# Kernel optimization log

Hardware: AMD Instinct MI355X
Metric: run time of the kernel (lower is better)

## Reference

```python
import jax, jax.numpy as jnp
import numpy as np

B, T, C, H = 8, 2048, 1024, 64

def setup_inputs() -> dict:
    key = jax.random.key(0)
    kx, kq, kk, kv = jax.random.split(key, 4)
    scale = 1.0 / np.sqrt(C)
    return {
        "x": jax.random.normal(kx, (B, T, C), dtype=jnp.float32),
        "Wq": jax.random.normal(kq, (C, H), dtype=jnp.float32) * scale,
        "Wk": jax.random.normal(kk, (C, H), dtype=jnp.float32) * scale,
        "Wv": jax.random.normal(kv, (C, H), dtype=jnp.float32) * scale,
    }

def reference(x, Wq, Wk, Wv):
    # q,k,v: [B,T,H]
    q = jnp.einsum('btc,ch->bth', x, Wq)
    k = jnp.einsum('btc,ch->bth', x, Wk)
    v = jnp.einsum('btc,ch->bth', x, Wv)
    scale = k.shape[-1] ** -0.5
    wei = jnp.einsum('bth,bsh->bts', q, k) * scale  # [B,T,T]
    causal = jnp.tril(jnp.ones((x.shape[1], x.shape[1]), dtype=bool))
    wei = jnp.where(causal, wei, -jnp.inf)
    wei = jax.nn.softmax(wei, axis=-1)
    out = jnp.einsum('bts,bsh->bth', wei, v)  # [B,T,H]
    return out
```

## Files before the change

### kernel.cpp

```cpp
#include <hip/hip_runtime.h>

#define B_ 8
#define T_ 2048
#define C_ 1024
#define H_ 64

typedef __bf16 bf16x8 __attribute__((ext_vector_type(8)));
typedef float  f32x4  __attribute__((ext_vector_type(4)));
typedef unsigned short u16x8 __attribute__((ext_vector_type(8)));

__device__ __forceinline__ unsigned short f2bf(float f) {
    unsigned u = __builtin_bit_cast(unsigned, f);
    u += 0x8000u;
    return (unsigned short)(u >> 16);
}

__device__ __forceinline__ float bf2f(unsigned short v) {
    unsigned u = ((unsigned)v) << 16;
    return __builtin_bit_cast(float, u);
}

__device__ __forceinline__ unsigned pack2(float lo, float hi) {
    unsigned a = __builtin_bit_cast(unsigned, lo) + 0x8000u;
    unsigned b = __builtin_bit_cast(unsigned, hi) + 0x8000u;
    return (a >> 16) | (b & 0xffff0000u);
}

union U8 { unsigned u32[4]; u16x8 v; };

__device__ __forceinline__ u16x8 cvt8(float4 f0, float4 f1) {
    U8 r;
    r.u32[0] = pack2(f0.x, f0.y);
    r.u32[1] = pack2(f0.z, f0.w);
    r.u32[2] = pack2(f1.x, f1.y);
    r.u32[3] = pack2(f1.z, f1.w);
    return r.v;
}

__device__ __forceinline__ bf16x8 load8_bf(const unsigned short* p) {
    return __builtin_bit_cast(bf16x8, *(const u16x8*)p);
}

__device__ __forceinline__ void gload_lds16(const float* g, float* l) {
    __builtin_amdgcn_global_load_lds(
        (const __attribute__((address_space(1))) unsigned int*)g,
        (__attribute__((address_space(3))) unsigned int*)l, 16, 0, 0);
}

__device__ __forceinline__ void stage_rows(const float* __restrict__ x,
                                           float* lbuf, size_t rbase,
                                           int ns, int lane, int half) {
#pragma unroll
    for (int q = 0; q < 8; q++) {
        int jj  = half * 8 + q;
        int j   = ns * 16 + jj;
        int row = j >> 2;
        int S0  = (j & 3) * 64;
        int g   = (S0 + lane) ^ (row & 7);
        gload_lds16(x + (rbase + row) * C_ + (size_t)g * 4,
                    lbuf + row * 1024 + S0 * 4);
    }
}


__global__ void cast_weights(const float* __restrict__ Wq,
                             const float* __restrict__ Wk,
                             const float* __restrict__ Wv,
                             unsigned short* __restrict__ Wtf) {
    int idx = blockIdx.x * blockDim.x + threadIdx.x;
    int n   = idx % 192;
    int c   = idx / 192;
    int w   = n >> 6;
    int h   = n & 63;
    const float* W = (w == 0) ? Wq : (w == 1) ? Wk : Wv;
    int nt = n >> 4, l16 = n & 15;
    int kk = c >> 5, quad = (c >> 3) & 3, j = c & 7;
    Wtf[(size_t)(nt * 32 + kk) * 512 + l16 * 32 + quad * 8 + j] =
        f2bf(W[(size_t)c * H_ + h]);
}

__global__ __launch_bounds__(256, 1) void qkv_proj(
        const float* __restrict__ x,
        const unsigned short* __restrict__ Wtf,
        unsigned short* __restrict__ Qf,
        unsigned short* __restrict__ Kf,
        unsigned short* __restrict__ Vf) {
    __shared__ __attribute__((aligned(16))) float Axs[2][16 * 1024];
    __shared__ __attribute__((aligned(16))) unsigned short E[3072];

    const int tid  = threadIdx.x;
    const int ns   = tid >> 6;
    const int lane = tid & 63;
    const int l16  = lane & 15;
    const int quad = lane >> 4;
    const size_t rblk = (size_t)blockIdx.x * 64;
    const int bb   = (int)(rblk >> 11);
    const int xsw  = l16 & 7;
    const unsigned short* wp = Wtf + (size_t)(ns * 3 * 32) * 512
                               + l16 * 32 + quad * 8;

    stage_rows(x, Axs[0], rblk, ns, lane, 0);
    stage_rows(x, Axs[0], rblk, ns, lane, 1);
    __syncthreads();

    for (int t = 0; t < 4; t++) {
        const float* Arow = &Axs[t & 1][l16 * 1024];
        float* bufN = &Axs[(t + 1) & 1][0];
        const size_t rnext = rblk + (size_t)(t + 1) * 16;

        f32x4 acc[3];
#pragma unroll
        for (int i = 0; i < 3; i++) acc[i] = (f32x4){0.f, 0.f, 0.f, 0.f};

#pragma unroll
        for (int kc = 0; kc < 4; kc++) {
            if (kc == 1 && t < 3) stage_rows(x, bufN, rnext, ns, lane, 0);
            if (kc == 2 && t < 3) stage_rows(x, bufN, rnext, ns, lane, 1);
#pragma unroll
            for (int k8 = 0; k8 < 8; k8++) {
                const int kk = kc * 8 + k8;
                int g0 = kk * 8 + quad * 2;
                float4 f0 = *(const float4*)(Arow + (size_t)((g0    ) ^ xsw) * 4);
                float4 f1 = *(const float4*)(Arow + (size_t)((g0 + 1) ^ xsw) * 4);
                bf16x8 a0 = __builtin_bit_cast(bf16x8, cvt8(f0, f1));
#pragma unroll
                for (int i = 0; i < 3; i++) {
                    bf16x8 b = load8_bf(wp + (size_t)(i * 32 + kk) * 512);
                    acc[i] = __builtin_amdgcn_mfma_f32_16x16x32_bf16(a0, b, acc[i], 0, 0, 0);
                }
            }
        }

        __syncthreads();

        const int tloc0  = (int)((rblk + (size_t)t * 16) & (T_ - 1));
        const int t16_0  = tloc0 >> 4;
        const int s32    = tloc0 >> 5;
        const int half16 = t16_0 & 1;

#pragma unroll
        for (int i = 0; i < 3; i++) {
            int nt = ns * 3 + i;
#pragma unroll
            for (int r = 0; r < 4; r++) {
                unsigned short bv = f2bf(acc[i][r]);
                int off;
                if (nt < 4) {
                    off = (nt >> 1) * 512 + (quad * 4 + r) * 32 +
                          ((nt & 1) * 2 + (l16 >> 3)) * 8 + (l16 & 7);
                } else if (nt < 8) {
                    int nk = nt - 4;
                    off = 1024 + (nk >> 1) * 512 + (quad * 4 + r) * 32 +
                          ((nk & 1) * 2 + (l16 >> 3)) * 8 + (l16 & 7);
                } else {
                    int ht = nt - 8;
                    off = 2048 + ht * 256 + l16 * 16 + quad * 4 + r;
                }
                E[off] = bv;
            }
        }
        __syncthreads();

        {
            int ch = tid >> 6;
            int g  = tid & 63;
            unsigned short* dst = (ch < 2) ? Qf : Kf;
            int part = ch & 1;
            dst += ((size_t)(bb * 128 + t16_0) * 2 + part) * 512;
            *(u16x8*)(dst + g * 8) = *(const u16x8*)(&E[ch * 512 + g * 8]);
        }
        if (tid < 128) {
            int ht   = tid >> 5;
            int rr   = tid & 31;
            int l16v = rr >> 1;
            int hh   = rr & 1;
            unsigned short* dst = Vf + ((size_t)(bb * 64 + s32) * 4 + ht) * 512
                                  + l16v * 32 + half16 * 16 + hh * 8;
            *(u16x8*)dst = *(const u16x8*)(&E[2048 + ht * 256 + l16v * 16 + hh * 8]);
        }
    }
}

#define PROW 33
#define OMS2 66

__global__ __launch_bounds__(256) void attn(
        const unsigned short* __restrict__ Qf,
        const unsigned short* __restrict__ Kf,
        const unsigned short* __restrict__ Vf,
        float* __restrict__ out) {
    __shared__ unsigned int ps_[4 * 32 * PROW];
    __shared__ unsigned short Om_[4 * 32 * OMS2];
    __shared__ float mred_[4][32];
    __shared__ float lred_[4][32];

    const int tid  = threadIdx.x;
    const int wave = tid >> 6;
    const int lane = tid & 63;
    const int l16  = lane & 15;
    const int quad = lane >> 4;
    const int b    = blockIdx.x & 7;
    const int qt32 = blockIdx.x >> 3;
    const int q0   = qt32 * 32;
    const int tdiag = qt32 >> 1;

    const int loff = l16 * 32 + quad * 8;

    bf16x8 qf[2][2];
#pragma unroll
    for (int qg = 0; qg < 2; qg++) {
        const unsigned short* Qfb = Qf + (size_t)((b * 128 + qt32 * 2 + qg) * 2) * 512;
        qf[qg][0] = load8_bf(Qfb + loff);
        qf[qg][1] = load8_bf(Qfb + 512 + loff);
    }

    f32x4 o[8];
#pragma unroll
    for (int i = 0; i < 8; i++) o[i] = (f32x4){0.f, 0.f, 0.f, 0.f};
    float m_run[2] = {-1e30f, -1e30f}, l_run[2] = {0.f, 0.f};

    const float scale = 0.125f;
    const unsigned short* Kfb = Kf + (size_t)b * 128 * 1024;
    const unsigned short* Vfb = Vf + (size_t)b * 64 * 2048;
    unsigned int* Pw = &ps_[wave * 32 * PROW];

    for (int t = wave; t <= tdiag; t += 4) {
        bf16x8 vf[8];
#pragma unroll
        for (int ks = 0; ks < 2; ks++)
#pragma unroll
            for (int ht = 0; ht < 4; ht++)
                vf[ht * 2 + ks] = load8_bf(
                    Vfb + ((size_t)(t * 2 + ks) * 4 + ht) * 512 + loff);

        f32x4 s[2][4];
#pragma unroll
        for (int nt = 0; nt < 4; nt++) {
            const unsigned short* kp = Kfb + (size_t)(t * 4 + nt) * 1024;
            bf16x8 kf0 = load8_bf(kp + loff);
            bf16x8 kf1 = load8_bf(kp + 512 + loff);
#pragma unroll
            for (int qg = 0; qg < 2; qg++) {
                f32x4 z = (f32x4){0.f, 0.f, 0.f, 0.f};
                z = __builtin_amdgcn_mfma_f32_16x16x32_bf16(kf0, qf[qg][0], z, 0, 0, 0);
                z = __builtin_amdgcn_mfma_f32_16x16x32_bf16(kf1, qf[qg][1], z, 0, 0, 0);
                s[qg][nt] = z;
            }
        }

#pragma unroll
        for (int qg = 0; qg < 2; qg++)
#pragma unroll
            for (int nt = 0; nt < 4; nt++)
#pragma unroll
                for (int r = 0; r < 4; r++) s[qg][nt][r] *= scale;

        if (t == tdiag) {
#pragma unroll
            for (int qg = 0; qg < 2; qg++) {
                int q = q0 + qg * 16 + l16;
#pragma unroll
                for (int nt = 0; nt < 4; nt++)
#pragma unroll
                    for (int r = 0; r < 4; r++) {
                        int key = t * 64 + nt * 16 + quad * 4 + r;
                        if (key > q) s[qg][nt][r] = -1e30f;
                    }
            }
        }

#pragma unroll
        for (int qg = 0; qg < 2; qg++) {
            float m0 = fmaxf(fmaxf(s[qg][0][0], s[qg][0][1]), fmaxf(s[qg][0][2], s[qg][0][3]));
            float m1 = fmaxf(fmaxf(s[qg][1][0], s[qg][1][1]), fmaxf(s[qg][1][2], s[qg][1][3]));
            float m2 = fmaxf(fmaxf(s[qg][2][0], s[qg][2][1]), fmaxf(s[qg][2][2], s[qg][2][3]));
            float m3 = fmaxf(fmaxf(s[qg][3][0], s[qg][3][1]), fmaxf(s[qg][3][2], s[qg][3][3]));
            float mx = fmaxf(fmaxf(m0, m1), fmaxf(m2, m3));
            mx = fmaxf(mx, __shfl_xor(mx, 16));
            mx = fmaxf(mx, __shfl_xor(mx, 32));
            const float m_new = fmaxf(m_run[qg], mx);
            const float alpha = __expf(m_run[qg] - m_new);
            m_run[qg] = m_new;

            float rs = 0.f;
#pragma unroll
            for (int nt = 0; nt < 4; nt++) {
#pragma unroll
                for (int i = 0; i < 2; i++) {
                    float p0 = __expf(s[qg][nt][2 * i]     - m_new);
                    float p1 = __expf(s[qg][nt][2 * i + 1] - m_new);
                    rs += p0 + p1;
                    Pw[(qg * 16 + l16) * PROW + nt * 8 + quad * 2 + i] = pack2(p0, p1);
                }
            }
            rs += __shfl_xor(rs, 16);
            rs += __shfl_xor(rs, 32);
            l_run[qg] = l_run[qg] * alpha + rs;

#pragma unroll
            for (int ht = 0; ht < 4; ht++)
#pragma unroll
                for (int r = 0; r < 4; r++) o[qg * 4 + ht][r] *= alpha;
        }

#pragma unroll
        for (int ks = 0; ks < 2; ks++) {
#pragma unroll
            for (int qg = 0; qg < 2; qg++) {
                bf16x8 pB = __builtin_bit_cast(bf16x8,
                    *(const u16x8*)(&Pw[(qg * 16 + l16) * PROW + ks * 16 + quad * 4]));
#pragma unroll
                for (int ht = 0; ht < 4; ht++)
                    o[qg * 4 + ht] = __builtin_amdgcn_mfma_f32_16x16x32_bf16(
                        vf[ht * 2 + ks], pB, o[qg * 4 + ht], 0, 0, 0);
            }
        }
    }

#pragma unroll
    for (int qg = 0; qg < 2; qg++) {
#pragma unroll
        for (int ht = 0; ht < 4; ht++)
#pragma unroll
            for (int r = 0; r < 4; r++)
                Om_[(wave * 32 + qg * 16 + l16) * OMS2 + ht * 16 + quad * 4 + r] =
                    f2bf(o[qg * 4 + ht][r]);
        if (quad == 0) {
            mred_[wave][qg * 16 + l16] = m_run[qg];
            lred_[wave][qg * 16 + l16] = l_run[qg];
        }
    }
    __syncthreads();

    const int hcol = tid & 63;
    const int qr0  = tid >> 6;
#pragma unroll
    for (int qq = 0; qq < 8; qq++) {
        const int q = qr0 + qq * 4;
        float M = -1e30f;
#pragma unroll
        for (int w = 0; w < 4; w++) M = fmaxf(M, mred_[w][q]);
        float lt = 0.f, ov = 0.f;
#pragma unroll
        for (int w = 0; w < 4; w++) {
            float e = __expf(mred_[w][q] - M);
            lt += e * lred_[w][q];
            ov += e * bf2f(Om_[(w * 32 + q) * OMS2 + hcol]);
        }
        out[((size_t)b * T_ + q0 + q) * H_ + hcol] = ov / lt;
    }
}

extern "C" void kernel_launch(void* const* d_in, const int* in_sizes, int n_in,
                              void* d_out, int out_size, void* d_ws, size_t ws_size,
                              hipStream_t stream) {
    const float* x  = (const float*)d_in[0];
    const float* Wq = (const float*)d_in[1];
    const float* Wk = (const float*)d_in[2];
    const float* Wv = (const float*)d_in[3];
    float* out = (float*)d_out;

    unsigned short* Qf  = (unsigned short*)d_ws;
    unsigned short* Kf  = Qf + (size_t)B_ * T_ * H_;
    unsigned short* Vf  = Kf + (size_t)B_ * T_ * H_;
    unsigned short* Wtf = Vf + (size_t)B_ * T_ * H_;

    cast_weights<<<(192 * C_) / 256, 256, 0, stream>>>(Wq, Wk, Wv, Wtf);
    qkv_proj<<<B_ * T_ / 64, 256, 0, stream>>>(x, Wtf, Qf, Kf, Vf);
    attn<<<B_ * (T_ / 32), 256, 0, stream>>>(Qf, Kf, Vf, out);
}
```

Baseline: 149.3 us.

## Restructure QKV projection: 12 waves with register-resident weights and bf16 LDS staging

The projection kernel now runs 768 threads (12 waves), each owning one 16-column output tile, and holds its full 32-step weight fragment in registers instead of reloading weights from global memory every k-step. x rows are staged as fp32 into LDS, converted once to swizzled bf16 in a double-buffered LDS array, and the MFMA loop reads bf16 directly, which removes the per-wave redundant fp32-to-bf16 conversion. This adds register pressure (32 bf16x8 fragments per thread) and an extra conversion pass with a barrier. Occupancy changes under the new launch bounds.

```diff
diff --git a/kernel.cpp b/kernel.cpp
--- a/kernel.cpp
+++ b/kernel.cpp
@@ -45,21 +45,6 @@
     __builtin_amdgcn_global_load_lds(
         (const __attribute__((address_space(1))) unsigned int*)g,
         (__attribute__((address_space(3))) unsigned int*)l, 16, 0, 0);
-}
-
-__device__ __forceinline__ void stage_rows(const float* __restrict__ x,
-                                           float* lbuf, size_t rbase,
-                                           int ns, int lane, int half) {
-#pragma unroll
-    for (int q = 0; q < 8; q++) {
-        int jj  = half * 8 + q;
-        int j   = ns * 16 + jj;
-        int row = j >> 2;
-        int S0  = (j & 3) * 64;
-        int g   = (S0 + lane) ^ (row & 7);
-        gload_lds16(x + (rbase + row) * C_ + (size_t)g * 4,
-                    lbuf + row * 1024 + S0 * 4);
-    }
 }
 
 
@@ -79,71 +64,97 @@
         f2bf(W[(size_t)c * H_ + h]);
 }
 
-__global__ __launch_bounds__(256, 1) void qkv_proj(
+__global__ __launch_bounds__(768, 3) void qkv_proj(
         const float* __restrict__ x,
         const unsigned short* __restrict__ Wtf,
         unsigned short* __restrict__ Qf,
         unsigned short* __restrict__ Kf,
         unsigned short* __restrict__ Vf) {
-    __shared__ __attribute__((aligned(16))) float Axs[2][16 * 1024];
+    __shared__ __attribute__((aligned(16))) float F[16 * 1024];
+    __shared__ __attribute__((aligned(16))) unsigned short A2[2][16 * 1024];
     __shared__ __attribute__((aligned(16))) unsigned short E[3072];
 
     const int tid  = threadIdx.x;
-    const int ns   = tid >> 6;
+    const int w    = tid >> 6;
     const int lane = tid & 63;
     const int l16  = lane & 15;
     const int quad = lane >> 4;
     const size_t rblk = (size_t)blockIdx.x * 64;
     const int bb   = (int)(rblk >> 11);
+    const int loff = l16 * 32 + quad * 8;
     const int xsw  = l16 & 7;
-    const unsigned short* wp = Wtf + (size_t)(ns * 3 * 32) * 512
-                               + l16 * 32 + quad * 8;
-
-    stage_rows(x, Axs[0], rblk, ns, lane, 0);
-    stage_rows(x, Axs[0], rblk, ns, lane, 1);
+
+    bf16x8 Bf[32];
+#pragma unroll
+    for (int kk = 0; kk < 32; kk++)
+        Bf[kk] = load8_bf(Wtf + (size_t)(w * 32 + kk) * 512 + loff);
+
+    if (w < 8) {
+#pragma unroll
+        for (int q = 0; q < 8; q++) {
+            int j   = w * 8 + q;
+            int row = j >> 2;
+            int G0  = (j & 3) * 64;
+            gload_lds16(x + (rblk + row) * C_ + (size_t)(G0 + lane) * 4,
+                        &F[row * 1024 + G0 * 4]);
+        }
+    }
     __syncthreads();
 
+    if (tid < 512) {
+#pragma unroll
+        for (int jj = 0; jj < 4; jj++) {
+            int p = jj * 512 + tid;
+            int r = p >> 7, s = p & 127;
+            float4 f0 = *(const float4*)(&F[p * 8]);
+            float4 f1 = *(const float4*)(&F[p * 8 + 4]);
+            *(u16x8*)(&A2[0][r * 1024 + (s ^ (r & 7)) * 8]) = cvt8(f0, f1);
+        }
+    }
+    __syncthreads();
+
     for (int t = 0; t < 4; t++) {
-        const float* Arow = &Axs[t & 1][l16 * 1024];
-        float* bufN = &Axs[(t + 1) & 1][0];
-        const size_t rnext = rblk + (size_t)(t + 1) * 16;
-
-        f32x4 acc[3];
-#pragma unroll
-        for (int i = 0; i < 3; i++) acc[i] = (f32x4){0.f, 0.f, 0.f, 0.f};
-
-#pragma unroll
-        for (int kc = 0; kc < 4; kc++) {
-            if (kc == 1 && t < 3) stage_rows(x, bufN, rnext, ns, lane, 0);
-            if (kc == 2 && t < 3) stage_rows(x, bufN, rnext, ns, lane, 1);
-#pragma unroll
-            for (int k8 = 0; k8 < 8; k8++) {
-                const int kk = kc * 8 + k8;
-                int g0 = kk * 8 + quad * 2;
-                float4 f0 = *(const float4*)(Arow + (size_t)((g0    ) ^ xsw) * 4);
-                float4 f1 = *(const float4*)(Arow + (size_t)((g0 + 1) ^ xsw) * 4);
-                bf16x8 a0 = __builtin_bit_cast(bf16x8, cvt8(f0, f1));
-#pragma unroll
-                for (int i = 0; i < 3; i++) {
-                    bf16x8 b = load8_bf(wp + (size_t)(i * 32 + kk) * 512);
-                    acc[i] = __builtin_amdgcn_mfma_f32_16x16x32_bf16(a0, b, acc[i], 0, 0, 0);
-                }
-            }
-        }
-
+        if (t < 3 && w < 8) {
+            const size_t rnext = rblk + (size_t)(t + 1) * 16;
+#pragma unroll
+            for (int q = 0; q < 8; q++) {
+                int j   = w * 8 + q;
+                int row = j >> 2;
+                int G0  = (j & 3) * 64;
+                gload_lds16(x + (rnext + row) * C_ + (size_t)(G0 + lane) * 4,
+                            &F[row * 1024 + G0 * 4]);
+            }
+        }
+
+        const unsigned short* Ar = &A2[t & 1][l16 * 1024];
+        f32x4 acc = (f32x4){0.f, 0.f, 0.f, 0.f};
+#pragma unroll
+        for (int kk = 0; kk < 32; kk++) {
+            bf16x8 a0 = load8_bf(Ar + ((kk * 4 + quad) ^ xsw) * 8);
+            acc = __builtin_amdgcn_mfma_f32_16x16x32_bf16(a0, Bf[kk], acc, 0, 0, 0);
+        }
         __syncthreads();
+
+        if (t < 3 && tid < 512) {
+#pragma unroll
+            for (int jj = 0; jj < 4; jj++) {
+                int p = jj * 512 + tid;
+                int r = p >> 7, s = p & 127;
+                float4 f0 = *(const float4*)(&F[p * 8]);
+                float4 f1 = *(const float4*)(&F[p * 8 + 4]);
+                *(u16x8*)(&A2[(t + 1) & 1][r * 1024 + (s ^ (r & 7)) * 8]) = cvt8(f0, f1);
+            }
+        }
 
         const int tloc0  = (int)((rblk + (size_t)t * 16) & (T_ - 1));
         const int t16_0  = tloc0 >> 4;
         const int s32    = tloc0 >> 5;
         const int half16 = t16_0 & 1;
-
-#pragma unroll
-        for (int i = 0; i < 3; i++) {
-            int nt = ns * 3 + i;
+        {
+            const int nt = w;
 #pragma unroll
             for (int r = 0; r < 4; r++) {
-                unsigned short bv = f2bf(acc[i][r]);
+                unsigned short bv = f2bf(acc[r]);
                 int off;
                 if (nt < 4) {
                     off = (nt >> 1) * 512 + (quad * 4 + r) * 32 +
@@ -161,17 +172,17 @@
         }
         __syncthreads();
 
-        {
+        if (tid < 256) {
             int ch = tid >> 6;
             int g  = tid & 63;
             unsigned short* dst = (ch < 2) ? Qf : Kf;
             int part = ch & 1;
             dst += ((size_t)(bb * 128 + t16_0) * 2 + part) * 512;
             *(u16x8*)(dst + g * 8) = *(const u16x8*)(&E[ch * 512 + g * 8]);
-        }
-        if (tid < 128) {
-            int ht   = tid >> 5;
-            int rr   = tid & 31;
+        } else if (tid < 384) {
+            int rr2  = tid - 256;
+            int ht   = rr2 >> 5;
+            int rr   = rr2 & 31;
             int l16v = rr >> 1;
             int hh   = rr & 1;
             unsigned short* dst = Vf + ((size_t)(bb * 64 + s32) * 4 + ht) * 512
@@ -366,6 +377,6 @@
     unsigned short* Wtf = Vf + (size_t)B_ * T_ * H_;
 
     cast_weights<<<(192 * C_) / 256, 256, 0, stream>>>(Wq, Wk, Wv, Wtf);
-    qkv_proj<<<B_ * T_ / 64, 256, 0, stream>>>(x, Wtf, Qf, Kf, Vf);
+    qkv_proj<<<B_ * T_ / 64, 768, 0, stream>>>(x, Wtf, Qf, Kf, Vf);
     attn<<<B_ * (T_ / 32), 256, 0, stream>>>(Qf, Kf, Vf, out);
 }
```

Result: slower. 161.4 us (+8.1%).
